# Performance work log

Measured on AMD Instinct MI355X. Metric: run time of the kernel, lower is better.

Reference implementation:

```python
import jax, jax.numpy as jnp
import numpy as np

IN_DIM = 3
GRID_LEVEL = 7
FEAT_DIMS = 2
HIDDEN = 128
BOUND = 1.0
W0_SINE = 56.0  # n_levels**feature_dims - n_levels = 8**2 - 8
N = 131072


def setup_inputs() -> dict:
    key = jax.random.key(0)
    ks = jax.random.split(key, 10)
    return {
        "in_pos": jax.random.uniform(ks[0], (N, IN_DIM), jnp.float32, -1.0, 1.0),
        "grid_feats": jax.random.uniform(ks[1], (N, IN_DIM + GRID_LEVEL * FEAT_DIMS), jnp.float32),
        "ffn_A": jax.random.normal(ks[2], (GRID_LEVEL, FEAT_DIMS, HIDDEN), jnp.float32) * 5.0,
        "ffn_sigma": jnp.ones((GRID_LEVEL,), jnp.float32),
        "W0": jax.random.uniform(ks[3], (HIDDEN, IN_DIM), jnp.float32, -1.0 / IN_DIM, 1.0 / IN_DIM),
        "b0": jax.random.uniform(ks[4], (HIDDEN,), jnp.float32, -1.0 / IN_DIM, 1.0 / IN_DIM),
        "W_mid": jax.random.uniform(ks[5], (GRID_LEVEL, HIDDEN, HIDDEN), jnp.float32) * (2.0 * np.sqrt(6.0 / HIDDEN) / W0_SINE) - np.sqrt(6.0 / HIDDEN) / W0_SINE,
        "b_mid": jnp.zeros((GRID_LEVEL, HIDDEN), jnp.float32),
        "W_high": jax.random.uniform(ks[6], (GRID_LEVEL, HIDDEN, HIDDEN), jnp.float32) * (2.0 * np.sqrt(6.0 / HIDDEN) / W0_SINE) - np.sqrt(6.0 / HIDDEN) / W0_SINE,
        "b_high": jnp.zeros((GRID_LEVEL, HIDDEN), jnp.float32),
    }


def reference(in_pos, grid_feats, ffn_A, ffn_sigma, W0, b0, W_mid, b_mid, W_high, b_high):
    x = in_pos / BOUND                     # [N, 3], in [-1, 1]
    pos01 = (in_pos + BOUND) / (2.0 * BOUND)  # [N, 3], in [0, 1]

    # grid branch: slice off the first in_dim columns, reshape to [L, N, F]
    gx = grid_feats[..., IN_DIM:].reshape(-1, GRID_LEVEL, FEAT_DIMS).transpose(1, 0, 2)
    A = ffn_A * ffn_sigma[:, None, None]   # [L, F, H]
    grid_x = jnp.sin(jnp.einsum('lnf,lfh->lnh', gx, (2.0 * jnp.pi) * A))  # [L, N, H]

    # first SIREN layer
    x = jnp.sin(W0_SINE * (x @ W0.T + b0))  # [N, H]

    def step(carry, layer):
        x, buf = carry
        Wm, bm, Wh, bh, g = layer
        x = jnp.sin(W0_SINE * (x @ Wm.T + bm))
        x = g + x                                  # residual add of grid features
        buf = buf + jnp.sin(W0_SINE * (x @ Wh.T + bh))  # high-freq accumulation
        return (x, buf), None

    buf0 = jnp.zeros((x.shape[0], HIDDEN), x.dtype)
    (_, buf), _ = jax.lax.scan(step, (x, buf0), (W_mid, b_mid, W_high, b_high, grid_x))

    return jnp.concatenate([pos01, buf / GRID_LEVEL], axis=-1)  # [N, 3 + 128]
```

## Files before the change

### kernel.cpp

```cpp
#include <hip/hip_runtime.h>
#include <hip/hip_bf16.h>


typedef __bf16 bf16_t;
typedef __attribute__((ext_vector_type(8))) __bf16 bf16x8;
typedef __attribute__((ext_vector_type(16))) float f32x16;

#define C56R 8.9126768f
#define INV7 0.14285714285714285f

#define OFF_WMHI 0
#define OFF_WMLO 229376
#define OFF_WHHI 458752
#define OFF_CBM  688128
#define OFF_CBH  691712
#define OFF_AP   695296
#define OFF_C0   702464

__device__ __forceinline__ float sin_rev(float r) {
  float fn = __builtin_rintf(r + r);
  float t  = __builtin_fmaf(fn, -0.5f, r);
  int   k  = (int)fn;
  float t2 = t * t;
  float p  = __builtin_fmaf(t2, 42.058693f, -76.705859f);
  p = __builtin_fmaf(t2, p, 81.605249f);
  p = __builtin_fmaf(t2, p, -41.341702f);
  p = __builtin_fmaf(t2, p, 6.2831853f);
  float sres = t * p;
  sres = __uint_as_float(__float_as_uint(sres) ^ ((unsigned)k << 31));
  return sres;
}

__global__ void ffb_prep(const float* __restrict__ ffnA, const float* __restrict__ sigma,
                         const float* __restrict__ b0,
                         const float* __restrict__ Wm, const float* __restrict__ bm,
                         const float* __restrict__ Wh, const float* __restrict__ bh,
                         unsigned char* __restrict__ ws) {
  int i = blockIdx.x * 256 + threadIdx.x;
  bf16_t* wmhi = (bf16_t*)(ws + OFF_WMHI);
  bf16_t* wmlo = (bf16_t*)(ws + OFF_WMLO);
  bf16_t* whhi = (bf16_t*)(ws + OFF_WHHI);
  float*  cbm  = (float*)(ws + OFF_CBM);
  float*  cbh  = (float*)(ws + OFF_CBH);
  float*  ap   = (float*)(ws + OFF_AP);
  float*  c0   = (float*)(ws + OFF_C0);
  if (i < 7 * 128 * 128) {
    float w = Wm[i];
    bf16_t h = (bf16_t)w;
    wmhi[i] = h;
    wmlo[i] = (bf16_t)(w - (float)h);
    whhi[i] = (bf16_t)Wh[i];
  }
  if (i < 896)  { cbm[i] = C56R * bm[i]; cbh[i] = C56R * bh[i]; }
  if (i < 1792) { ap[i] = ffnA[i] * sigma[i >> 8]; }
  if (i < 128)  { c0[i] = C56R * b0[i]; }
}

__launch_bounds__(256, 2)
__global__ void ffb_main(const float* __restrict__ pos,
                         const float* __restrict__ gfeat,
                         const float* __restrict__ W0,
                         const unsigned char* __restrict__ ws,
                         float* __restrict__ out) {
  __shared__ __align__(16) unsigned char smem[69632 + 128 * 14 * 4];
  bf16_t* Xhi = (bf16_t*)smem;
  bf16_t* Xlo = (bf16_t*)(smem + 34816);
  float*  GF  = (float*)(smem + 69632);
  float*  OST = (float*)smem;

  const int tid    = threadIdx.x;
  const int base_n = blockIdx.x << 7;
  const int w   = tid >> 6;
  const int L   = tid & 63;
  const int s   = L & 31;
  const int h5  = L >> 5;
  const int col = (w << 5) + s;

  const bf16_t* __restrict__ WMHI = (const bf16_t*)(ws + OFF_WMHI);
  const bf16_t* __restrict__ WMLO = (const bf16_t*)(ws + OFF_WMLO);
  const bf16_t* __restrict__ WHHI = (const bf16_t*)(ws + OFF_WHHI);
  const float*  __restrict__ CBM  = (const float*)(ws + OFF_CBM);
  const float*  __restrict__ CBH  = (const float*)(ws + OFF_CBH);
  const float*  __restrict__ AP   = (const float*)(ws + OFF_AP);
  const float*  __restrict__ C0   = (const float*)(ws + OFF_C0);

  for (int i = tid; i < 128 * 14; i += 256) {
    int n = i / 14, l = i - n * 14;
    GF[i] = gfeat[(size_t)(base_n + n) * 17 + 3 + l];
  }

  {
    int nl = tid >> 1;
    int n  = base_n + nl;
    int hstart = (tid & 1) << 6;
    float p0 = pos[n*3+0], p1 = pos[n*3+1], p2 = pos[n*3+2];
    #pragma unroll 8
    for (int h = hstart; h < hstart + 64; h += 2) {
      float d0 = p0*W0[h*3+0] + p1*W0[h*3+1] + p2*W0[h*3+2];
      float d1 = p0*W0[h*3+3] + p1*W0[h*3+4] + p2*W0[h*3+5];
      float x0 = sin_rev(__builtin_fmaf(d0, C56R, C0[h]));
      float x1 = sin_rev(__builtin_fmaf(d1, C56R, C0[h+1]));
      bf16_t hi0 = (bf16_t)x0, hi1 = (bf16_t)x1;
      Xhi[nl*136 + h]     = hi0;
      Xhi[nl*136 + h + 1] = hi1;
      Xlo[nl*136 + h]     = (bf16_t)(x0 - (float)hi0);
      Xlo[nl*136 + h + 1] = (bf16_t)(x1 - (float)hi1);
    }
  }
  __syncthreads();

  f32x16 buf[4];
  #pragma unroll
  for (int mt = 0; mt < 4; ++mt)
    #pragma unroll
    for (int r = 0; r < 16; ++r) buf[mt][r] = 0.f;

  for (int it = 0; it < 8; ++it) {
    if (it > 0) {
      f32x16 acc[4];
      #pragma unroll
      for (int mt = 0; mt < 4; ++mt)
        #pragma unroll
        for (int r = 0; r < 16; ++r) acc[mt][r] = 0.f;
      const bf16_t* whh = WHHI + ((it - 1) << 14) + (col << 7);
      #pragma unroll 2
      for (int kc = 0; kc < 8; ++kc) {
        const int kof = (kc << 4) + (h5 << 3);
        bf16x8 Bhh = *(const bf16x8*)(whh + kof);
        #pragma unroll
        for (int mt = 0; mt < 4; ++mt) {
          const int row = (mt << 5) + s;
          bf16x8 Ahi = *(const bf16x8*)(&Xhi[row*136 + kof]);
          bf16x8 Alo = *(const bf16x8*)(&Xlo[row*136 + kof]);
          acc[mt] = __builtin_amdgcn_mfma_f32_32x32x16_bf16(Ahi, Bhh, acc[mt], 0, 0, 0);
          acc[mt] = __builtin_amdgcn_mfma_f32_32x32x16_bf16(Alo, Bhh, acc[mt], 0, 0, 0);
        }
      }
      const float cbh_l = CBH[((it - 1) << 7) + col];
      #pragma unroll
      for (int mt = 0; mt < 4; ++mt)
        #pragma unroll
        for (int r = 0; r < 16; ++r)
          buf[mt][r] += __builtin_amdgcn_sinf(__builtin_fmaf(acc[mt][r], C56R, cbh_l));
    }

    if (it < 7) {
      f32x16 acc[4];
      #pragma unroll
      for (int mt = 0; mt < 4; ++mt)
        #pragma unroll
        for (int r = 0; r < 16; ++r) acc[mt][r] = 0.f;
      const bf16_t* wmh = WMHI + (it << 14) + (col << 7);
      const bf16_t* wml = WMLO + (it << 14) + (col << 7);
      #pragma unroll 2
      for (int kc = 0; kc < 8; ++kc) {
        const int kof = (kc << 4) + (h5 << 3);
        bf16x8 Bmh = *(const bf16x8*)(wmh + kof);
        bf16x8 Bml = *(const bf16x8*)(wml + kof);
        #pragma unroll
        for (int mt = 0; mt < 4; ++mt) {
          const int row = (mt << 5) + s;
          bf16x8 Ahi = *(const bf16x8*)(&Xhi[row*136 + kof]);
          bf16x8 Alo = *(const bf16x8*)(&Xlo[row*136 + kof]);
          acc[mt] = __builtin_amdgcn_mfma_f32_32x32x16_bf16(Ahi, Bmh, acc[mt], 0, 0, 0);
          acc[mt] = __builtin_amdgcn_mfma_f32_32x32x16_bf16(Ahi, Bml, acc[mt], 0, 0, 0);
          acc[mt] = __builtin_amdgcn_mfma_f32_32x32x16_bf16(Alo, Bmh, acc[mt], 0, 0, 0);
        }
      }
      __syncthreads();
      const float cbm_l = CBM[(it << 7) + col];
      const float ap0 = AP[(it << 8) + col];
      const float ap1 = AP[(it << 8) + 128 + col];
      #pragma unroll
      for (int mt = 0; mt < 4; ++mt) {
        #pragma unroll
        for (int r = 0; r < 16; ++r) {
          const int rowl = (mt << 5) + (r & 3) + ((r >> 2) << 3) + (h5 << 2);
          float gx0 = GF[rowl * 14 + (it << 1)];
          float gx1 = GF[rowl * 14 + (it << 1) + 1];
          float grev = __builtin_fmaf(gx1, ap1, gx0 * ap0);
          float xv = sin_rev(grev) + sin_rev(__builtin_fmaf(acc[mt][r], C56R, cbm_l));
          bf16_t hi = (bf16_t)xv;
          Xhi[rowl*136 + col] = hi;
          Xlo[rowl*136 + col] = (bf16_t)(xv - (float)hi);
        }
      }
      __syncthreads();
    }
  }

  __syncthreads();
  #pragma unroll
  for (int mt = 0; mt < 4; ++mt) {
    #pragma unroll
    for (int r = 0; r < 16; ++r) {
      const int rowl = (mt << 5) + (r & 3) + ((r >> 2) << 3) + (h5 << 2);
      OST[rowl * 131 + 3 + col] = buf[mt][r] * INV7;
    }
  }
  if (tid < 128) {
    int n = base_n + tid;
    OST[tid * 131 + 0] = (pos[n*3+0] + 1.f) * 0.5f;
    OST[tid * 131 + 1] = (pos[n*3+1] + 1.f) * 0.5f;
    OST[tid * 131 + 2] = (pos[n*3+2] + 1.f) * 0.5f;
  }
  __syncthreads();
  {
    float* outp = out + (size_t)base_n * 131;
    for (int i = tid; i < 128 * 131; i += 256) outp[i] = OST[i];
  }
}

extern "C" void kernel_launch(void* const* d_in, const int* in_sizes, int n_in,
                              void* d_out, int out_size, void* d_ws, size_t ws_size,
                              hipStream_t stream) {
  (void)in_sizes; (void)n_in; (void)out_size; (void)ws_size;
  const float* pos   = (const float*)d_in[0];
  const float* gfeat = (const float*)d_in[1];
  const float* ffnA  = (const float*)d_in[2];
  const float* sigma = (const float*)d_in[3];
  const float* W0    = (const float*)d_in[4];
  const float* b0    = (const float*)d_in[5];
  const float* Wm    = (const float*)d_in[6];
  const float* bm    = (const float*)d_in[7];
  const float* Wh    = (const float*)d_in[8];
  const float* bh    = (const float*)d_in[9];
  float* out = (float*)d_out;
  unsigned char* ws = (unsigned char*)d_ws;

  hipLaunchKernelGGL(ffb_prep, dim3(448), dim3(256), 0, stream,
                     ffnA, sigma, b0, Wm, bm, Wh, bh, ws);
  hipLaunchKernelGGL(ffb_main, dim3(1024), dim3(256), 0, stream,
                     pos, gfeat, W0, ws, out);
}
```

Measured before the change: 315.0 us.

## Halve block tile to 64 rows, use hardware sine, drop lo-term in high branch

Each block now handles 64 points instead of 128, which halves the accumulator registers and shared memory so occupancy can rise to 4 blocks per CU, and the grid doubles. The polynomial software sine is replaced by the hardware v_sin instruction, with fract-based range reduction for the grid branch. The Xlo correction MFMA in the high-frequency layer is removed, and the output copy now uses float4 stores. The cost is lower sine accuracy at large arguments and a less exact high-branch matmul, plus more weight reloads per point.

Result: faster. 303.4 us (-3.7%).

```diff
diff --git a/kernel.cpp b/kernel.cpp
--- a/kernel.cpp
+++ b/kernel.cpp
@@ -4,6 +4,7 @@
 
 typedef __bf16 bf16_t;
 typedef __attribute__((ext_vector_type(8))) __bf16 bf16x8;
+typedef __attribute__((ext_vector_type(4))) float f32x4;
 typedef __attribute__((ext_vector_type(16))) float f32x16;
 
 #define C56R 8.9126768f
@@ -16,20 +17,6 @@
 #define OFF_CBH  691712
 #define OFF_AP   695296
 #define OFF_C0   702464
-
-__device__ __forceinline__ float sin_rev(float r) {
-  float fn = __builtin_rintf(r + r);
-  float t  = __builtin_fmaf(fn, -0.5f, r);
-  int   k  = (int)fn;
-  float t2 = t * t;
-  float p  = __builtin_fmaf(t2, 42.058693f, -76.705859f);
-  p = __builtin_fmaf(t2, p, 81.605249f);
-  p = __builtin_fmaf(t2, p, -41.341702f);
-  p = __builtin_fmaf(t2, p, 6.2831853f);
-  float sres = t * p;
-  sres = __uint_as_float(__float_as_uint(sres) ^ ((unsigned)k << 31));
-  return sres;
-}
 
 __global__ void ffb_prep(const float* __restrict__ ffnA, const float* __restrict__ sigma,
                          const float* __restrict__ b0,
@@ -56,20 +43,20 @@
   if (i < 128)  { c0[i] = C56R * b0[i]; }
 }
 
-__launch_bounds__(256, 2)
+__launch_bounds__(256, 4)
 __global__ void ffb_main(const float* __restrict__ pos,
                          const float* __restrict__ gfeat,
                          const float* __restrict__ W0,
                          const unsigned char* __restrict__ ws,
                          float* __restrict__ out) {
-  __shared__ __align__(16) unsigned char smem[69632 + 128 * 14 * 4];
+  __shared__ __align__(16) unsigned char smem[38400];
   bf16_t* Xhi = (bf16_t*)smem;
-  bf16_t* Xlo = (bf16_t*)(smem + 34816);
-  float*  GF  = (float*)(smem + 69632);
+  bf16_t* Xlo = (bf16_t*)(smem + 17408);
+  float*  GF  = (float*)(smem + 34816);
   float*  OST = (float*)smem;
 
   const int tid    = threadIdx.x;
-  const int base_n = blockIdx.x << 7;
+  const int base_n = blockIdx.x << 6;
   const int w   = tid >> 6;
   const int L   = tid & 63;
   const int s   = L & 31;
@@ -84,70 +71,63 @@
   const float*  __restrict__ AP   = (const float*)(ws + OFF_AP);
   const float*  __restrict__ C0   = (const float*)(ws + OFF_C0);
 
-  for (int i = tid; i < 128 * 14; i += 256) {
+  for (int i = tid; i < 64 * 14; i += 256) {
     int n = i / 14, l = i - n * 14;
     GF[i] = gfeat[(size_t)(base_n + n) * 17 + 3 + l];
   }
 
   {
-    int nl = tid >> 1;
-    int n  = base_n + nl;
-    int hstart = (tid & 1) << 6;
+    int rl = tid >> 2;
+    int n  = base_n + rl;
+    int hstart = (tid & 3) << 5;
     float p0 = pos[n*3+0], p1 = pos[n*3+1], p2 = pos[n*3+2];
     #pragma unroll 8
-    for (int h = hstart; h < hstart + 64; h += 2) {
-      float d0 = p0*W0[h*3+0] + p1*W0[h*3+1] + p2*W0[h*3+2];
-      float d1 = p0*W0[h*3+3] + p1*W0[h*3+4] + p2*W0[h*3+5];
-      float x0 = sin_rev(__builtin_fmaf(d0, C56R, C0[h]));
-      float x1 = sin_rev(__builtin_fmaf(d1, C56R, C0[h+1]));
-      bf16_t hi0 = (bf16_t)x0, hi1 = (bf16_t)x1;
-      Xhi[nl*136 + h]     = hi0;
-      Xhi[nl*136 + h + 1] = hi1;
-      Xlo[nl*136 + h]     = (bf16_t)(x0 - (float)hi0);
-      Xlo[nl*136 + h + 1] = (bf16_t)(x1 - (float)hi1);
+    for (int h = hstart; h < hstart + 32; ++h) {
+      float d = p0*W0[h*3+0] + p1*W0[h*3+1] + p2*W0[h*3+2];
+      float x0 = __builtin_amdgcn_sinf(__builtin_fmaf(d, C56R, C0[h]));
+      bf16_t hi = (bf16_t)x0;
+      Xhi[rl*136 + h] = hi;
+      Xlo[rl*136 + h] = (bf16_t)(x0 - (float)hi);
     }
   }
   __syncthreads();
 
-  f32x16 buf[4];
+  f32x16 buf[2];
   #pragma unroll
-  for (int mt = 0; mt < 4; ++mt)
+  for (int mt = 0; mt < 2; ++mt)
     #pragma unroll
     for (int r = 0; r < 16; ++r) buf[mt][r] = 0.f;
 
   for (int it = 0; it < 8; ++it) {
     if (it > 0) {
-      f32x16 acc[4];
-      #pragma unroll
-      for (int mt = 0; mt < 4; ++mt)
+      f32x16 acc[2];
+      #pragma unroll
+      for (int mt = 0; mt < 2; ++mt)
         #pragma unroll
         for (int r = 0; r < 16; ++r) acc[mt][r] = 0.f;
       const bf16_t* whh = WHHI + ((it - 1) << 14) + (col << 7);
-      #pragma unroll 2
+      #pragma unroll 4
       for (int kc = 0; kc < 8; ++kc) {
         const int kof = (kc << 4) + (h5 << 3);
         bf16x8 Bhh = *(const bf16x8*)(whh + kof);
         #pragma unroll
-        for (int mt = 0; mt < 4; ++mt) {
-          const int row = (mt << 5) + s;
-          bf16x8 Ahi = *(const bf16x8*)(&Xhi[row*136 + kof]);
-          bf16x8 Alo = *(const bf16x8*)(&Xlo[row*136 + kof]);
+        for (int mt = 0; mt < 2; ++mt) {
+          bf16x8 Ahi = *(const bf16x8*)(&Xhi[((mt << 5) + s)*136 + kof]);
           acc[mt] = __builtin_amdgcn_mfma_f32_32x32x16_bf16(Ahi, Bhh, acc[mt], 0, 0, 0);
-          acc[mt] = __builtin_amdgcn_mfma_f32_32x32x16_bf16(Alo, Bhh, acc[mt], 0, 0, 0);
         }
       }
       const float cbh_l = CBH[((it - 1) << 7) + col];
       #pragma unroll
-      for (int mt = 0; mt < 4; ++mt)
+      for (int mt = 0; mt < 2; ++mt)
         #pragma unroll
         for (int r = 0; r < 16; ++r)
           buf[mt][r] += __builtin_amdgcn_sinf(__builtin_fmaf(acc[mt][r], C56R, cbh_l));
     }
 
     if (it < 7) {
-      f32x16 acc[4];
-      #pragma unroll
-      for (int mt = 0; mt < 4; ++mt)
+      f32x16 acc[2];
+      #pragma unroll
+      for (int mt = 0; mt < 2; ++mt)
         #pragma unroll
         for (int r = 0; r < 16; ++r) acc[mt][r] = 0.f;
       const bf16_t* wmh = WMHI + (it << 14) + (col << 7);
@@ -158,10 +138,9 @@
         bf16x8 Bmh = *(const bf16x8*)(wmh + kof);
         bf16x8 Bml = *(const bf16x8*)(wml + kof);
         #pragma unroll
-        for (int mt = 0; mt < 4; ++mt) {
-          const int row = (mt << 5) + s;
-          bf16x8 Ahi = *(const bf16x8*)(&Xhi[row*136 + kof]);
-          bf16x8 Alo = *(const bf16x8*)(&Xlo[row*136 + kof]);
+        for (int mt = 0; mt < 2; ++mt) {
+          bf16x8 Ahi = *(const bf16x8*)(&Xhi[((mt << 5) + s)*136 + kof]);
+          bf16x8 Alo = *(const bf16x8*)(&Xlo[((mt << 5) + s)*136 + kof]);
           acc[mt] = __builtin_amdgcn_mfma_f32_32x32x16_bf16(Ahi, Bmh, acc[mt], 0, 0, 0);
           acc[mt] = __builtin_amdgcn_mfma_f32_32x32x16_bf16(Ahi, Bml, acc[mt], 0, 0, 0);
           acc[mt] = __builtin_amdgcn_mfma_f32_32x32x16_bf16(Alo, Bmh, acc[mt], 0, 0, 0);
@@ -172,14 +151,16 @@
       const float ap0 = AP[(it << 8) + col];
       const float ap1 = AP[(it << 8) + 128 + col];
       #pragma unroll
-      for (int mt = 0; mt < 4; ++mt) {
+      for (int mt = 0; mt < 2; ++mt) {
         #pragma unroll
         for (int r = 0; r < 16; ++r) {
           const int rowl = (mt << 5) + (r & 3) + ((r >> 2) << 3) + (h5 << 2);
           float gx0 = GF[rowl * 14 + (it << 1)];
           float gx1 = GF[rowl * 14 + (it << 1) + 1];
           float grev = __builtin_fmaf(gx1, ap1, gx0 * ap0);
-          float xv = sin_rev(grev) + sin_rev(__builtin_fmaf(acc[mt][r], C56R, cbm_l));
+          float sg = __builtin_amdgcn_sinf(__builtin_amdgcn_fractf(grev));
+          float sm = __builtin_amdgcn_sinf(__builtin_fmaf(acc[mt][r], C56R, cbm_l));
+          float xv = sg + sm;
           bf16_t hi = (bf16_t)xv;
           Xhi[rowl*136 + col] = hi;
           Xlo[rowl*136 + col] = (bf16_t)(xv - (float)hi);
@@ -191,14 +172,14 @@
 
   __syncthreads();
   #pragma unroll
-  for (int mt = 0; mt < 4; ++mt) {
+  for (int mt = 0; mt < 2; ++mt) {
     #pragma unroll
     for (int r = 0; r < 16; ++r) {
       const int rowl = (mt << 5) + (r & 3) + ((r >> 2) << 3) + (h5 << 2);
       OST[rowl * 131 + 3 + col] = buf[mt][r] * INV7;
     }
   }
-  if (tid < 128) {
+  if (tid < 64) {
     int n = base_n + tid;
     OST[tid * 131 + 0] = (pos[n*3+0] + 1.f) * 0.5f;
     OST[tid * 131 + 1] = (pos[n*3+1] + 1.f) * 0.5f;
@@ -206,8 +187,9 @@
   }
   __syncthreads();
   {
-    float* outp = out + (size_t)base_n * 131;
-    for (int i = tid; i < 128 * 131; i += 256) outp[i] = OST[i];
+    f32x4* outp = (f32x4*)(out + (size_t)base_n * 131);
+    const f32x4* ostv = (const f32x4*)OST;
+    for (int i = tid; i < 64 * 131 / 4; i += 256) outp[i] = ostv[i];
   }
 }
 
@@ -230,6 +212,6 @@
 
   hipLaunchKernelGGL(ffb_prep, dim3(448), dim3(256), 0, stream,
                      ffnA, sigma, b0, Wm, bm, Wh, bh, ws);
-  hipLaunchKernelGGL(ffb_main, dim3(1024), dim3(256), 0, stream,
+  hipLaunchKernelGGL(ffb_main, dim3(2048), dim3(256), 0, stream,
                      pos, gfeat, W0, ws, out);
 }
```

## Restructure SIREN kernel to register-resident activations with one wave per 32 points

Applied to the files above, without the earlier changes.

The kernel moves from 256-thread blocks holding 128 points' activations in LDS to 64-thread single-wave blocks of 32 points, with activations held in registers as MFMA B operands. The weights are pre-swizzled into MFMA fragment order and loaded straight from global memory. Activations are redistributed between half-waves with ds_bpermute instead of LDS round-trips and __syncthreads. The custom sin polynomial is replaced by hardware sinf, and the high-frequency GEMM drops the lo-part correction. This removes LDS traffic and barriers but re-reads weights per wave from cache, writes output uncoalesced, and lowers precision.

Result: slower. 428.3 us (+36.0%).

```diff
diff --git a/kernel.cpp b/kernel.cpp
--- a/kernel.cpp
+++ b/kernel.cpp
@@ -4,110 +4,131 @@
 
 typedef __bf16 bf16_t;
 typedef __attribute__((ext_vector_type(8))) __bf16 bf16x8;
+typedef __attribute__((ext_vector_type(4))) float f32x4;
 typedef __attribute__((ext_vector_type(16))) float f32x16;
 
 #define C56R 8.9126768f
 #define INV7 0.14285714285714285f
 
-#define OFF_WMHI 0
-#define OFF_WMLO 229376
-#define OFF_WHHI 458752
-#define OFF_CBM  688128
-#define OFF_CBH  691712
-#define OFF_AP   695296
-#define OFF_C0   702464
-
-__device__ __forceinline__ float sin_rev(float r) {
-  float fn = __builtin_rintf(r + r);
-  float t  = __builtin_fmaf(fn, -0.5f, r);
-  int   k  = (int)fn;
-  float t2 = t * t;
-  float p  = __builtin_fmaf(t2, 42.058693f, -76.705859f);
-  p = __builtin_fmaf(t2, p, 81.605249f);
-  p = __builtin_fmaf(t2, p, -41.341702f);
-  p = __builtin_fmaf(t2, p, 6.2831853f);
-  float sres = t * p;
-  sres = __uint_as_float(__float_as_uint(sres) ^ ((unsigned)k << 31));
-  return sres;
+#define OFF_WMF   0
+#define OFF_WMFLO 229376
+#define OFF_WHF   458752
+#define OFF_EPM   688128
+
+union ChunkU { bf16x8 v; unsigned int d[4]; };
+
+__device__ __forceinline__ unsigned short bfbits(float x) {
+  bf16_t b = (bf16_t)x;
+  return __builtin_bit_cast(unsigned short, b);
+}
+__device__ __forceinline__ float bf2f(unsigned short u) {
+  return __builtin_bit_cast(float, (unsigned int)u << 16);
+}
+__device__ __forceinline__ void pack2(float v0, float v1,
+                                      unsigned int& ph, unsigned int& pl) {
+  unsigned short h0 = bfbits(v0), h1 = bfbits(v1);
+  ph = (unsigned int)h0 | ((unsigned int)h1 << 16);
+  float l0 = v0 - bf2f(h0), l1 = v1 - bf2f(h1);
+  pl = (unsigned int)bfbits(l0) | ((unsigned int)bfbits(l1) << 16);
+}
+__device__ __forceinline__ void exch(const unsigned int P[8], int hf, int bpidx,
+                                     ChunkU& cA, ChunkU& cB) {
+  unsigned int t0 = hf ? P[0] : P[2];
+  unsigned int t1 = hf ? P[1] : P[3];
+  unsigned int t2 = hf ? P[4] : P[6];
+  unsigned int t3 = hf ? P[5] : P[7];
+  unsigned int r0 = (unsigned int)__builtin_amdgcn_ds_bpermute(bpidx, (int)t0);
+  unsigned int r1 = (unsigned int)__builtin_amdgcn_ds_bpermute(bpidx, (int)t1);
+  unsigned int r2 = (unsigned int)__builtin_amdgcn_ds_bpermute(bpidx, (int)t2);
+  unsigned int r3 = (unsigned int)__builtin_amdgcn_ds_bpermute(bpidx, (int)t3);
+  cA.d[0] = hf ? r0 : P[0];
+  cA.d[1] = hf ? r1 : P[1];
+  cA.d[2] = hf ? P[2] : r0;
+  cA.d[3] = hf ? P[3] : r1;
+  cB.d[0] = hf ? r2 : P[4];
+  cB.d[1] = hf ? r3 : P[5];
+  cB.d[2] = hf ? P[6] : r2;
+  cB.d[3] = hf ? P[7] : r3;
 }
 
 __global__ void ffb_prep(const float* __restrict__ ffnA, const float* __restrict__ sigma,
-                         const float* __restrict__ b0,
                          const float* __restrict__ Wm, const float* __restrict__ bm,
                          const float* __restrict__ Wh, const float* __restrict__ bh,
                          unsigned char* __restrict__ ws) {
   int i = blockIdx.x * 256 + threadIdx.x;
-  bf16_t* wmhi = (bf16_t*)(ws + OFF_WMHI);
-  bf16_t* wmlo = (bf16_t*)(ws + OFF_WMLO);
-  bf16_t* whhi = (bf16_t*)(ws + OFF_WHHI);
-  float*  cbm  = (float*)(ws + OFF_CBM);
-  float*  cbh  = (float*)(ws + OFF_CBH);
-  float*  ap   = (float*)(ws + OFF_AP);
-  float*  c0   = (float*)(ws + OFF_C0);
-  if (i < 7 * 128 * 128) {
-    float w = Wm[i];
+  bf16_t* wmf = (bf16_t*)(ws + OFF_WMF);
+  bf16_t* wml = (bf16_t*)(ws + OFF_WMFLO);
+  bf16_t* whf = (bf16_t*)(ws + OFF_WHF);
+  {
+    int j    = i & 7;
+    int lane = (i >> 3) & 63;
+    int kc   = (i >> 9) & 7;
+    int mt   = (i >> 12) & 3;
+    int it   = i >> 14;
+    int ho   = (mt << 5) + (lane & 31);
+    int hin  = (kc << 4) + ((lane >> 5) << 3) + j;
+    int src  = (it << 14) + (ho << 7) + hin;
+    float w  = Wm[src];
     bf16_t h = (bf16_t)w;
-    wmhi[i] = h;
-    wmlo[i] = (bf16_t)(w - (float)h);
-    whhi[i] = (bf16_t)Wh[i];
-  }
-  if (i < 896)  { cbm[i] = C56R * bm[i]; cbh[i] = C56R * bh[i]; }
-  if (i < 1792) { ap[i] = ffnA[i] * sigma[i >> 8]; }
-  if (i < 128)  { c0[i] = C56R * b0[i]; }
-}
-
-__launch_bounds__(256, 2)
+    wmf[i] = h;
+    wml[i] = (bf16_t)(w - (float)h);
+    whf[i] = (bf16_t)Wh[src];
+  }
+  if (i < 896) {
+    int r  = i & 15;
+    int mt = (i >> 4) & 3;
+    int hf = (i >> 6) & 1;
+    int it = i >> 7;
+    int h  = (mt << 5) + (r & 3) + ((r >> 2) << 3) + (hf << 2);
+    float sg = sigma[it];
+    f32x4 e;
+    e.x = ffnA[it * 256 + h] * sg;
+    e.y = ffnA[it * 256 + 128 + h] * sg;
+    e.z = C56R * bm[it * 128 + h];
+    e.w = C56R * bh[it * 128 + h];
+    ((f32x4*)(ws + OFF_EPM))[i] = e;
+  }
+}
+
+__launch_bounds__(64, 2)
 __global__ void ffb_main(const float* __restrict__ pos,
                          const float* __restrict__ gfeat,
                          const float* __restrict__ W0,
+                         const float* __restrict__ b0,
                          const unsigned char* __restrict__ ws,
                          float* __restrict__ out) {
-  __shared__ __align__(16) unsigned char smem[69632 + 128 * 14 * 4];
-  bf16_t* Xhi = (bf16_t*)smem;
-  bf16_t* Xlo = (bf16_t*)(smem + 34816);
-  float*  GF  = (float*)(smem + 69632);
-  float*  OST = (float*)smem;
-
-  const int tid    = threadIdx.x;
-  const int base_n = blockIdx.x << 7;
-  const int w   = tid >> 6;
-  const int L   = tid & 63;
-  const int s   = L & 31;
-  const int h5  = L >> 5;
-  const int col = (w << 5) + s;
-
-  const bf16_t* __restrict__ WMHI = (const bf16_t*)(ws + OFF_WMHI);
-  const bf16_t* __restrict__ WMLO = (const bf16_t*)(ws + OFF_WMLO);
-  const bf16_t* __restrict__ WHHI = (const bf16_t*)(ws + OFF_WHHI);
-  const float*  __restrict__ CBM  = (const float*)(ws + OFF_CBM);
-  const float*  __restrict__ CBH  = (const float*)(ws + OFF_CBH);
-  const float*  __restrict__ AP   = (const float*)(ws + OFF_AP);
-  const float*  __restrict__ C0   = (const float*)(ws + OFF_C0);
-
-  for (int i = tid; i < 128 * 14; i += 256) {
-    int n = i / 14, l = i - n * 14;
-    GF[i] = gfeat[(size_t)(base_n + n) * 17 + 3 + l];
-  }
-
-  {
-    int nl = tid >> 1;
-    int n  = base_n + nl;
-    int hstart = (tid & 1) << 6;
-    float p0 = pos[n*3+0], p1 = pos[n*3+1], p2 = pos[n*3+2];
-    #pragma unroll 8
-    for (int h = hstart; h < hstart + 64; h += 2) {
-      float d0 = p0*W0[h*3+0] + p1*W0[h*3+1] + p2*W0[h*3+2];
-      float d1 = p0*W0[h*3+3] + p1*W0[h*3+4] + p2*W0[h*3+5];
-      float x0 = sin_rev(__builtin_fmaf(d0, C56R, C0[h]));
-      float x1 = sin_rev(__builtin_fmaf(d1, C56R, C0[h+1]));
-      bf16_t hi0 = (bf16_t)x0, hi1 = (bf16_t)x1;
-      Xhi[nl*136 + h]     = hi0;
-      Xhi[nl*136 + h + 1] = hi1;
-      Xlo[nl*136 + h]     = (bf16_t)(x0 - (float)hi0);
-      Xlo[nl*136 + h + 1] = (bf16_t)(x1 - (float)hi1);
-    }
-  }
-  __syncthreads();
+  const int L  = threadIdx.x;
+  const int p  = L & 31;
+  const int hf = L >> 5;
+  const int bpidx  = ((L ^ 32) << 2);
+  const int n      = (blockIdx.x << 5) + p;
+
+  const bf16_t* __restrict__ WMF = (const bf16_t*)(ws + OFF_WMF);
+  const bf16_t* __restrict__ WML = (const bf16_t*)(ws + OFF_WMFLO);
+  const bf16_t* __restrict__ WHF = (const bf16_t*)(ws + OFF_WHF);
+  const f32x4*  __restrict__ EPM = (const f32x4*)(ws + OFF_EPM);
+  const float*  __restrict__ EPW = (const float*)(ws + OFF_EPM);
+
+  const float p0 = pos[n * 3 + 0], p1 = pos[n * 3 + 1], p2 = pos[n * 3 + 2];
+  if (hf == 0) {
+    out[n * 131 + 0] = (p0 + 1.f) * 0.5f;
+    out[n * 131 + 1] = (p1 + 1.f) * 0.5f;
+    out[n * 131 + 2] = (p2 + 1.f) * 0.5f;
+  }
+
+  ChunkU xh[8], xl[8];
+  #pragma unroll
+  for (int q = 0; q < 8; ++q) {
+    #pragma unroll
+    for (int jp = 0; jp < 4; ++jp) {
+      int h0 = (q << 4) + (hf << 3) + 2 * jp;
+      float d0 = __builtin_fmaf(p2, W0[h0*3+2], __builtin_fmaf(p1, W0[h0*3+1], p0 * W0[h0*3+0]));
+      float d1 = __builtin_fmaf(p2, W0[h0*3+5], __builtin_fmaf(p1, W0[h0*3+4], p0 * W0[h0*3+3]));
+      float v0 = __builtin_amdgcn_sinf(C56R * (d0 + b0[h0]));
+      float v1 = __builtin_amdgcn_sinf(C56R * (d1 + b0[h0 + 1]));
+      pack2(v0, v1, xh[q].d[jp], xl[q].d[jp]);
+    }
+  }
 
   f32x16 buf[4];
   #pragma unroll
@@ -122,26 +143,24 @@
       for (int mt = 0; mt < 4; ++mt)
         #pragma unroll
         for (int r = 0; r < 16; ++r) acc[mt][r] = 0.f;
-      const bf16_t* whh = WHHI + ((it - 1) << 14) + (col << 7);
-      #pragma unroll 2
+      const bf16_t* wb = WHF + ((it - 1) << 14) + (L << 3);
+      #pragma unroll
       for (int kc = 0; kc < 8; ++kc) {
-        const int kof = (kc << 4) + (h5 << 3);
-        bf16x8 Bhh = *(const bf16x8*)(whh + kof);
         #pragma unroll
         for (int mt = 0; mt < 4; ++mt) {
-          const int row = (mt << 5) + s;
-          bf16x8 Ahi = *(const bf16x8*)(&Xhi[row*136 + kof]);
-          bf16x8 Alo = *(const bf16x8*)(&Xlo[row*136 + kof]);
-          acc[mt] = __builtin_amdgcn_mfma_f32_32x32x16_bf16(Ahi, Bhh, acc[mt], 0, 0, 0);
-          acc[mt] = __builtin_amdgcn_mfma_f32_32x32x16_bf16(Alo, Bhh, acc[mt], 0, 0, 0);
-        }
-      }
-      const float cbh_l = CBH[((it - 1) << 7) + col];
-      #pragma unroll
-      for (int mt = 0; mt < 4; ++mt)
-        #pragma unroll
-        for (int r = 0; r < 16; ++r)
-          buf[mt][r] += __builtin_amdgcn_sinf(__builtin_fmaf(acc[mt][r], C56R, cbh_l));
+          bf16x8 f = *(const bf16x8*)(wb + (((mt << 3) + kc) << 9));
+          acc[mt] = __builtin_amdgcn_mfma_f32_32x32x16_bf16(f, xh[kc].v, acc[mt], 0, 0, 0);
+        }
+      }
+      const int ebase = ((((it - 1) << 1) + hf) << 2);
+      #pragma unroll
+      for (int mt = 0; mt < 4; ++mt) {
+        #pragma unroll
+        for (int r = 0; r < 16; ++r) {
+          float cbh = EPW[((ebase + mt) * 16 + r) * 4 + 3];
+          buf[mt][r] += __builtin_amdgcn_sinf(__builtin_fmaf(acc[mt][r], C56R, cbh));
+        }
+      }
     }
 
     if (it < 7) {
@@ -150,64 +169,50 @@
       for (int mt = 0; mt < 4; ++mt)
         #pragma unroll
         for (int r = 0; r < 16; ++r) acc[mt][r] = 0.f;
-      const bf16_t* wmh = WMHI + (it << 14) + (col << 7);
-      const bf16_t* wml = WMLO + (it << 14) + (col << 7);
-      #pragma unroll 2
+      const bf16_t* wh = WMF + (it << 14) + (L << 3);
+      const bf16_t* wl = WML + (it << 14) + (L << 3);
+      #pragma unroll
       for (int kc = 0; kc < 8; ++kc) {
-        const int kof = (kc << 4) + (h5 << 3);
-        bf16x8 Bmh = *(const bf16x8*)(wmh + kof);
-        bf16x8 Bml = *(const bf16x8*)(wml + kof);
         #pragma unroll
         for (int mt = 0; mt < 4; ++mt) {
-          const int row = (mt << 5) + s;
-          bf16x8 Ahi = *(const bf16x8*)(&Xhi[row*136 + kof]);
-          bf16x8 Alo = *(const bf16x8*)(&Xlo[row*136 + kof]);
-          acc[mt] = __builtin_amdgcn_mfma_f32_32x32x16_bf16(Ahi, Bmh, acc[mt], 0, 0, 0);
-          acc[mt] = __builtin_amdgcn_mfma_f32_32x32x16_bf16(Ahi, Bml, acc[mt], 0, 0, 0);
-          acc[mt] = __builtin_amdgcn_mfma_f32_32x32x16_bf16(Alo, Bmh, acc[mt], 0, 0, 0);
-        }
-      }
-      __syncthreads();
-      const float cbm_l = CBM[(it << 7) + col];
-      const float ap0 = AP[(it << 8) + col];
-      const float ap1 = AP[(it << 8) + 128 + col];
+          const int off = (((mt << 3) + kc) << 9);
+          bf16x8 fh = *(const bf16x8*)(wh + off);
+          bf16x8 fl = *(const bf16x8*)(wl + off);
+          acc[mt] = __builtin_amdgcn_mfma_f32_32x32x16_bf16(fh, xh[kc].v, acc[mt], 0, 0, 0);
+          acc[mt] = __builtin_amdgcn_mfma_f32_32x32x16_bf16(fl, xh[kc].v, acc[mt], 0, 0, 0);
+          acc[mt] = __builtin_amdgcn_mfma_f32_32x32x16_bf16(fh, xl[kc].v, acc[mt], 0, 0, 0);
+        }
+      }
+      const float g0 = gfeat[n * 17 + 3 + 2 * it];
+      const float g1 = gfeat[n * 17 + 4 + 2 * it];
+      const int ebase = (((it << 1) + hf) << 2);
       #pragma unroll
       for (int mt = 0; mt < 4; ++mt) {
-        #pragma unroll
-        for (int r = 0; r < 16; ++r) {
-          const int rowl = (mt << 5) + (r & 3) + ((r >> 2) << 3) + (h5 << 2);
-          float gx0 = GF[rowl * 14 + (it << 1)];
-          float gx1 = GF[rowl * 14 + (it << 1) + 1];
-          float grev = __builtin_fmaf(gx1, ap1, gx0 * ap0);
-          float xv = sin_rev(grev) + sin_rev(__builtin_fmaf(acc[mt][r], C56R, cbm_l));
-          bf16_t hi = (bf16_t)xv;
-          Xhi[rowl*136 + col] = hi;
-          Xlo[rowl*136 + col] = (bf16_t)(xv - (float)hi);
-        }
-      }
-      __syncthreads();
-    }
-  }
-
-  __syncthreads();
+        unsigned int Ph[8], Pl[8];
+        #pragma unroll
+        for (int rp = 0; rp < 8; ++rp) {
+          f32x4 e0 = EPM[(ebase + mt) * 16 + 2 * rp];
+          f32x4 e1 = EPM[(ebase + mt) * 16 + 2 * rp + 1];
+          float sg0 = __builtin_amdgcn_sinf(__builtin_amdgcn_fractf(__builtin_fmaf(g1, e0.y, g0 * e0.x)));
+          float sg1 = __builtin_amdgcn_sinf(__builtin_amdgcn_fractf(__builtin_fmaf(g1, e1.y, g0 * e1.x)));
+          float sm0 = __builtin_amdgcn_sinf(__builtin_fmaf(acc[mt][2*rp],   C56R, e0.z));
+          float sm1 = __builtin_amdgcn_sinf(__builtin_fmaf(acc[mt][2*rp+1], C56R, e1.z));
+          pack2(sg0 + sm0, sg1 + sm1, Ph[rp], Pl[rp]);
+        }
+        exch(Ph, hf, bpidx, xh[2*mt], xh[2*mt + 1]);
+        exch(Pl, hf, bpidx, xl[2*mt], xl[2*mt + 1]);
+      }
+    }
+  }
+
+  float* op = out + n * 131 + 3;
   #pragma unroll
   for (int mt = 0; mt < 4; ++mt) {
     #pragma unroll
     for (int r = 0; r < 16; ++r) {
-      const int rowl = (mt << 5) + (r & 3) + ((r >> 2) << 3) + (h5 << 2);
-      OST[rowl * 131 + 3 + col] = buf[mt][r] * INV7;
-    }
-  }
-  if (tid < 128) {
-    int n = base_n + tid;
-    OST[tid * 131 + 0] = (pos[n*3+0] + 1.f) * 0.5f;
-    OST[tid * 131 + 1] = (pos[n*3+1] + 1.f) * 0.5f;
-    OST[tid * 131 + 2] = (pos[n*3+2] + 1.f) * 0.5f;
-  }
-  __syncthreads();
-  {
-    float* outp = out + (size_t)base_n * 131;
-    for (int i = tid; i < 128 * 131; i += 256) outp[i] = OST[i];
+      const int h = (mt << 5) + (r & 3) + ((r >> 2) << 3) + (hf << 2);
+      op[h] = buf[mt][r] * INV7;
+    }
   }
 }
 
@@ -229,7 +234,7 @@
   unsigned char* ws = (unsigned char*)d_ws;
 
   hipLaunchKernelGGL(ffb_prep, dim3(448), dim3(256), 0, stream,
-                     ffnA, sigma, b0, Wm, bm, Wh, bh, ws);
-  hipLaunchKernelGGL(ffb_main, dim3(1024), dim3(256), 0, stream,
-                     pos, gfeat, W0, ws, out);
-}
+                     ffnA, sigma, Wm, bm, Wh, bh, ws);
+  hipLaunchKernelGGL(ffb_main, dim3(4096), dim3(64), 0, stream,
+                     pos, gfeat, W0, b0, ws, out);
+}
```
